# Kernel optimization log

Hardware: AMD Instinct MI355X
Metric: run time of the kernel (lower is better)

The kernel has to match this reference:

```python
import jax, jax.numpy as jnp
import numpy as np

NUM_RELATIONS = 8
NUM_BASES = 4
IN_CH, HID, OUT_CH = 128, 64, 64
N_NODES, N_EDGES = 50000, 500000


def rgcn_conv(x, edge_src, edge_dst, edge_type, basis, comp, root, bias):
    """PyG RGCNConv with basis decomposition and per-relation mean aggregation.
    basis: [B, in, out], comp: [R, B], root: [in, out], bias: [out].
    W_r = sum_b comp[r, b] * basis[b]; msg_e = x[src_e] @ W_{type_e};
    aggregate mean over incoming edges per (node, relation), sum over relations,
    then add root transform and bias.
    """
    n = x.shape[0]
    out_dim = basis.shape[2]
    # Project once through all bases: [N, B, out]  (cheap: B=4)
    h = jnp.einsum('ni,bio->nbo', x, basis)
    # Per-edge message: contract gathered basis features with per-edge comp coeffs
    msg = jnp.einsum('eb,ebo->eo', comp[edge_type], h[edge_src])  # [E, out]
    # Mean aggregation per (dst, relation): segment id = dst*R + relation
    seg = edge_dst * NUM_RELATIONS + edge_type
    sums = jax.ops.segment_sum(msg, seg, num_segments=n * NUM_RELATIONS)
    cnt = jax.ops.segment_sum(jnp.ones((msg.shape[0], 1), msg.dtype), seg,
                              num_segments=n * NUM_RELATIONS)
    mean = sums / jnp.maximum(cnt, 1.0)
    agg = mean.reshape(n, NUM_RELATIONS, out_dim).sum(axis=1)
    return agg + x @ root + bias


def setup_inputs() -> dict:
    key = jax.random.key(0)
    ks = jax.random.split(key, 12)
    s1 = 1.0 / np.sqrt(IN_CH)
    s2 = 1.0 / np.sqrt(HID)
    return {
        'x': jax.random.normal(ks[0], (N_NODES, IN_CH), jnp.float32),
        'edge_index': jax.random.randint(ks[1], (2, N_EDGES), 0, N_NODES, jnp.int64),
        'edge_type': jax.random.randint(ks[2], (N_EDGES,), 0, NUM_RELATIONS, jnp.int64),
        'basis1': jax.random.normal(ks[3], (NUM_BASES, IN_CH, HID), jnp.float32) * s1,
        'comp1': jax.random.normal(ks[4], (NUM_RELATIONS, NUM_BASES), jnp.float32) * 0.5,
        'root1': jax.random.normal(ks[5], (IN_CH, HID), jnp.float32) * s1,
        'bias1': jnp.zeros((HID,), jnp.float32),
        'basis2': jax.random.normal(ks[6], (NUM_BASES, HID, OUT_CH), jnp.float32) * s2,
        'comp2': jax.random.normal(ks[7], (NUM_RELATIONS, NUM_BASES), jnp.float32) * 0.5,
        'root2': jax.random.normal(ks[8], (HID, OUT_CH), jnp.float32) * s2,
        'bias2': jnp.zeros((OUT_CH,), jnp.float32),
    }


def reference(x, edge_index, edge_type, basis1, comp1, root1, bias1,
              basis2, comp2, root2, bias2):
    src, dst = edge_index[0], edge_index[1]
    h = rgcn_conv(x, src, dst, edge_type, basis1, comp1, root1, bias1)
    h = jax.nn.relu(h)
    out = rgcn_conv(h, src, dst, edge_type, basis2, comp2, root2, bias2)
    return out
```

## Files before the change

### kernel.cpp

```cpp
#include <hip/hip_runtime.h>
#include <cstddef>

#define NREL 8
#define SCAN_TILE 4096

typedef __bf16 bf16x8 __attribute__((ext_vector_type(8)));
typedef float f32x4 __attribute__((ext_vector_type(4)));
typedef unsigned short ushort_t;

__device__ __forceinline__ unsigned f2bf_u(float f) {
    unsigned u = __float_as_uint(f);
    u += 0x7FFFu + ((u >> 16) & 1u);
    return u >> 16;
}
__device__ __forceinline__ short f2bf(float f) { return (short)f2bf_u(f); }
__device__ __forceinline__ int pack2bf(float lo, float hi) {
    return (int)(f2bf_u(lo) | (f2bf_u(hi) << 16));
}
__device__ __forceinline__ float bfval(unsigned short g) {
    return __uint_as_float((unsigned)g << 16);
}

__global__ __launch_bounds__(256) void zero_kernel(int4* __restrict__ p, int n16,
                                                   int* __restrict__ offsN, int E)
{
    int i = blockIdx.x * 256 + threadIdx.x;
    if (i < n16) p[i] = make_int4(0, 0, 0, 0);
    if (i == 0) *offsN = E;
}

template<int K>
__device__ __forceinline__ void wfrag_body(const float* __restrict__ basis,
                                           const float* __restrict__ root,
                                           const float* __restrict__ comp,
                                           short* __restrict__ Wf, int tid)
{
    constexpr int NK = K / 32;
    int lane = tid & 63, slot = tid >> 6;
    int ks = slot % NK, t = slot / NK;
    int kg = lane >> 4, lr = lane & 15;
    int k0 = ks * 32 + kg * 8;
    union { short s[8]; int4 v; } u;
#pragma unroll
    for (int e = 0; e < 8; ++e) {
        int k = k0 + e;
        float v;
        if (t < 32) {
            int rr = t >> 2, ch = (t & 3) * 16 + lr;
            v = comp[rr * 4 + 0] * basis[((size_t)0 * K + k) * 64 + ch]
              + comp[rr * 4 + 1] * basis[((size_t)1 * K + k) * 64 + ch]
              + comp[rr * 4 + 2] * basis[((size_t)2 * K + k) * 64 + ch]
              + comp[rr * 4 + 3] * basis[((size_t)3 * K + k) * 64 + ch];
        } else {
            v = root[(size_t)k * 64 + (t - 32) * 16 + lr];
        }
        u.s[e] = f2bf(v);
    }
    *(int4*)(Wf + (size_t)tid * 8) = u.v;
}

__device__ __forceinline__ void afrag_body128(const float* __restrict__ x,
                                              short* __restrict__ xf, int N, int tid)
{
    int lane = tid & 63, slot = tid >> 6;
    int ks = slot & 3, rt = slot >> 2;
    int kg = lane >> 4, lr = lane & 15;
    int row = rt * 16 + lr, k = ks * 32 + kg * 8;
    union { short s[8]; int4 v; } u;
    if (row < N) {
        const float* xp = x + (size_t)row * 128 + k;
        float4 a = *(const float4*)xp;
        float4 b = *(const float4*)(xp + 4);
        u.s[0] = f2bf(a.x); u.s[1] = f2bf(a.y); u.s[2] = f2bf(a.z); u.s[3] = f2bf(a.w);
        u.s[4] = f2bf(b.x); u.s[5] = f2bf(b.y); u.s[6] = f2bf(b.z); u.s[7] = f2bf(b.w);
    } else {
        u.v = make_int4(0, 0, 0, 0);
    }
    *(int4*)(xf + (size_t)tid * 8) = u.v;
}

__global__ __launch_bounds__(256) void prep_hist_kernel(
    const int* __restrict__ dstp, const int* __restrict__ et, int* __restrict__ cnt8,
    const float* __restrict__ basis1, const float* __restrict__ root1,
    const float* __restrict__ comp1,  const float* __restrict__ basis2,
    const float* __restrict__ root2,  const float* __restrict__ comp2,
    const float* __restrict__ x,
    short* __restrict__ Wf1, short* __restrict__ Wf2, short* __restrict__ xf1,
    int E, int N, int NT, int HB)
{
    int b = blockIdx.x;
    if (b < HB) {
        int e = b * 256 + threadIdx.x;
        if (e < E) atomicAdd(&cnt8[dstp[e] * NREL + et[e]], 1);
        return;
    }
    b -= HB;
    if (b < 36) { wfrag_body<128>(basis1, root1, comp1, Wf1, b * 256 + threadIdx.x); return; }
    b -= 36;
    if (b < 18) { wfrag_body<64>(basis2, root2, comp2, Wf2, b * 256 + threadIdx.x); return; }
    b -= 18;
    int tid = b * 256 + threadIdx.x;
    if (tid < NT * 256) afrag_body128(x, xf1, N, tid);
}

__global__ __launch_bounds__(256) void scan_part(const int* __restrict__ cnt8,
                                                 int* __restrict__ tsum, int n)
{
    int base = blockIdx.x * SCAN_TILE;
    int s = 0;
    for (int i = threadIdx.x; i < SCAN_TILE; i += 256) {
        int idx = base + i;
        if (idx < n) {
            int4 a = ((const int4*)cnt8)[idx * 2];
            int4 b = ((const int4*)cnt8)[idx * 2 + 1];
            s += a.x + a.y + a.z + a.w + b.x + b.y + b.z + b.w;
        }
    }
    for (int d = 1; d < 64; d <<= 1) s += __shfl_xor(s, d, 64);
    __shared__ int ws[4];
    if ((threadIdx.x & 63) == 0) ws[threadIdx.x >> 6] = s;
    __syncthreads();
    if (threadIdx.x == 0) tsum[blockIdx.x] = ws[0] + ws[1] + ws[2] + ws[3];
}

__global__ __launch_bounds__(256) void scan_final(const int* __restrict__ cnt8,
                                                  const int* __restrict__ tsum,
                                                  int* __restrict__ offs, int n)
{
    const int lane = threadIdx.x & 63, wid = threadIdx.x >> 6;
    int tbase = 0;
    for (int i = 0; i < blockIdx.x; ++i) tbase += tsum[i];
    int base = blockIdx.x * SCAN_TILE + threadIdx.x * 16;
    int v[16]; int s = 0;
#pragma unroll
    for (int j = 0; j < 16; ++j) {
        int idx = base + j;
        int dv = 0;
        if (idx < n) {
            int4 a = ((const int4*)cnt8)[idx * 2];
            int4 b = ((const int4*)cnt8)[idx * 2 + 1];
            dv = a.x + a.y + a.z + a.w + b.x + b.y + b.z + b.w;
        }
        v[j] = dv; s += dv;
    }
    int inc = s;
    for (int d = 1; d < 64; d <<= 1) {
        int t = __shfl_up(inc, d, 64);
        if (lane >= d) inc += t;
    }
    __shared__ int wsum[4];
    if (lane == 63) wsum[wid] = inc;
    __syncthreads();
    int run = tbase + (inc - s);
    for (int k = 0; k < wid; ++k) run += wsum[k];
#pragma unroll
    for (int j = 0; j < 16; ++j) {
        int idx = base + j;
        if (idx < n) offs[idx] = run;
        run += v[j];
    }
}

__global__ __launch_bounds__(256) void scatter_kernel(const int* __restrict__ src,
                                                      const int* __restrict__ dst,
                                                      const int* __restrict__ et,
                                                      const int* __restrict__ offs,
                                                      int* __restrict__ cursor,
                                                      const int* __restrict__ cnt8,
                                                      int2* __restrict__ edgeP,
                                                      ushort_t* __restrict__ edgeD, int E)
{
    int e = blockIdx.x * 256 + threadIdx.x;
    if (e >= E) return;
    int d = dst[e], r = et[e], s = src[e];
    int c = cnt8[d * NREL + r];
    float inv = 1.0f / (float)(c > 1 ? c : 1);
    int pos = offs[d] + atomicAdd(&cursor[d], 1);
    edgeP[pos] = make_int2(s * NREL + r, __float_as_int(inv));
    edgeD[pos] = (ushort_t)d;
}

template<int K>
__global__ __launch_bounds__(256) void gemm_mfma(const short* __restrict__ xf,
                                                 const short* __restrict__ Wf,
                                                 const float* __restrict__ bias,
                                                 short* __restrict__ hr,
                                                 short* __restrict__ yb,
                                                 int N, int gblk)
{
    constexpr int NK = K / 32;
    __shared__ short lds[12 * NK * 512];

    const int w = threadIdx.x >> 6, lane = threadIdx.x & 63;
    const int kg = lane >> 4, lr = lane & 15;
    const int g0 = blockIdx.y * 3;

    {
        const int4* gsrc = (const int4*)(Wf + (size_t)g0 * 4 * NK * 512);
        int4* ldst = (int4*)lds;
        for (int i = threadIdx.x; i < 12 * NK * 64; i += 256)
            ldst[i] = gsrc[i];
    }

    float b0 = bias[lr], b1 = bias[16 + lr], b2 = bias[32 + lr], b3 = bias[48 + lr];

    __syncthreads();

    for (int bx = blockIdx.x; bx < gblk; bx += gridDim.x) {
        const int rt = bx * 4 + w;

        bf16x8 afrag[NK];
        const short* ap = xf + ((size_t)rt * NK * 64 + lane) * 8;
#pragma unroll
        for (int ks = 0; ks < NK; ++ks)
            afrag[ks] = *(const bf16x8*)(ap + ks * 512);

        f32x4 acc[12];
#pragma unroll
        for (int t = 0; t < 12; ++t) acc[t] = (f32x4){0.f, 0.f, 0.f, 0.f};

#pragma unroll
        for (int tt = 0; tt < 12; ++tt) {
#pragma unroll
            for (int ks = 0; ks < NK; ++ks) {
                bf16x8 bfrag = *(const bf16x8*)(lds + (tt * NK + ks) * 512 + lane * 8);
                acc[tt] = __builtin_amdgcn_mfma_f32_16x16x32_bf16(afrag[ks], bfrag,
                                                                  acc[tt], 0, 0, 0);
            }
        }

        const int drow0 = rt * 16 + kg * 4;
#pragma unroll
        for (int r = 0; r < 4; ++r) {
            int dr = drow0 + r;
            if (dr >= N) break;
#pragma unroll
            for (int gg = 0; gg < 3; ++gg) {
                int g = g0 + gg;
                if (g < 8) {
                    int u0 = pack2bf(acc[gg * 4 + 0][r], acc[gg * 4 + 1][r]);
                    int u1 = pack2bf(acc[gg * 4 + 2][r], acc[gg * 4 + 3][r]);
                    *(int2*)(hr + (size_t)dr * 512 + g * 64 + lr * 4) = make_int2(u0, u1);
                } else {
                    int u0 = pack2bf(acc[gg * 4 + 0][r] + b0, acc[gg * 4 + 1][r] + b1);
                    int u1 = pack2bf(acc[gg * 4 + 2][r] + b2, acc[gg * 4 + 3][r] + b3);
                    *(int2*)(yb + (size_t)dr * 64 + lr * 4) = make_int2(u0, u1);
                }
            }
        }
    }
}

__global__ __launch_bounds__(256) void agg_chunk_kernel(
    const int2* __restrict__ edgeP, const ushort_t* __restrict__ edgeD,
    const short* __restrict__ hr, float* __restrict__ aggF, int E)
{
    const int w = threadIdx.x >> 6, l = threadIdx.x & 63;
    const int base = (blockIdx.x * 4 + w) * 16;
    if (base >= E) return;
    const int nv = min(16, E - base);

    int idx = base + (l & 15);
    if (idx >= E) idx = E - 1;
    int2 pl = edgeP[idx];
    int dl = (int)edgeD[idx];

    const unsigned short* hp = (const unsigned short*)hr;

    int g[16];
#pragma unroll
    for (int j = 0; j < 16; ++j) {
        int srj = __shfl(pl.x, j);
        g[j] = hp[(size_t)srj * 64 + l];
    }

    float acc = 0.f;
#pragma unroll
    for (int j = 0; j < 16; ++j) {
        if (j >= nv) break;
        float invj = __uint_as_float(__shfl(pl.y, j));
        acc = fmaf(bfval((unsigned short)g[j]), invj, acc);
        int dcur = __shfl(dl, j);
        int dnxt = __shfl(dl, (j + 1) & 15);
        if (j == nv - 1 || dnxt != dcur) {
            unsafeAtomicAdd(&aggF[(size_t)dcur * 64 + l], acc);
            acc = 0.f;
        }
    }
}

template<bool BF16OUT>
__global__ __launch_bounds__(256) void agg_fin_kernel(const float* __restrict__ aggF,
                                                      const short* __restrict__ yb,
                                                      float* __restrict__ outF,
                                                      short* __restrict__ outB, int N)
{
    int i = blockIdx.x * 256 + threadIdx.x;
    if (i >= N * 64) return;
    int dst = i >> 6, l = i & 63;
    float v = aggF[i] + bfval(((const ushort_t*)yb)[i]);
    int tc = (l & 3) * 16 + (l >> 2);
    if (BF16OUT) {
        int rt2 = dst >> 4, lr2 = dst & 15;
        int ks2 = tc >> 5, kg2 = (tc >> 3) & 3, e2 = tc & 7;
        outB[(((size_t)rt2 * 2 + ks2) * 64 + kg2 * 16 + lr2) * 8 + e2] =
            f2bf(fmaxf(v, 0.f));
    } else {
        outF[(size_t)dst * 64 + tc] = v;
    }
}

extern "C" void kernel_launch(void* const* d_in, const int* in_sizes, int n_in,
                              void* d_out, int out_size, void* d_ws, size_t ws_size,
                              hipStream_t stream)
{
    const float* x      = (const float*)d_in[0];
    const int*   ei     = (const int*)d_in[1];
    const int*   et     = (const int*)d_in[2];
    const float* basis1 = (const float*)d_in[3];
    const float* comp1  = (const float*)d_in[4];
    const float* root1  = (const float*)d_in[5];
    const float* bias1  = (const float*)d_in[6];
    const float* basis2 = (const float*)d_in[7];
    const float* comp2  = (const float*)d_in[8];
    const float* root2  = (const float*)d_in[9];
    const float* bias2  = (const float*)d_in[10];
    float* out = (float*)d_out;

    const int N = in_sizes[0] / 128;
    const int E = in_sizes[2];
    const int* src  = ei;
    const int* dstp = ei + E;

    const int gblk = (N + 63) / 64;
    const int NT   = gblk * 4;
    const int HB   = (E + 255) / 256;

    char* p = (char*)d_ws;
    auto carve = [&](size_t bytes) -> char* {
        char* q = p; p += (bytes + 255) & ~(size_t)255; return q;
    };
    int*   cursor  = (int*)carve((size_t)N * 4);
    int*   cnt8    = (int*)carve((size_t)N * NREL * 4);
    float* aggF1   = (float*)carve((size_t)N * 64 * 4);
    float* aggF2   = (float*)carve((size_t)N * 64 * 4);
    char*  zend    = p;
    int*   offs    = (int*)carve((size_t)(N + 1) * 4);
    int*   tsum    = (int*)carve(256 * 4);
    int2*  edgeP   = (int2*)carve((size_t)E * 8);
    ushort_t* edgeD = (ushort_t*)carve((size_t)E * 2);
    short* Wf1     = (short*)carve((size_t)36 * 4 * 64 * 8 * 2);
    short* Wf2     = (short*)carve((size_t)36 * 2 * 64 * 8 * 2);
    short* yb      = (short*)carve((size_t)N * 64 * 2);
    short* xf1     = (short*)carve((size_t)NT * 4 * 64 * 8 * 2);
    short* xf2     = (short*)carve((size_t)NT * 2 * 64 * 8 * 2);
    short* hr      = (short*)carve((size_t)N * 512 * 2);

    const int zn16 = (int)((zend - (char*)cursor) / 16);
    const int ntiles = (N + SCAN_TILE - 1) / SCAN_TILE;
    const int CHB = (E + 63) / 64;
    const int FB  = (N * 64 + 255) / 256;

    zero_kernel<<<(zn16 + 255) / 256, 256, 0, stream>>>((int4*)cursor, zn16, offs + N, E);

    prep_hist_kernel<<<HB + 36 + 18 + NT, 256, 0, stream>>>(
        dstp, et, cnt8, basis1, root1, comp1, basis2, root2, comp2, x,
        Wf1, Wf2, xf1, E, N, NT, HB);

    scan_part<<<ntiles, 256, 0, stream>>>(cnt8, tsum, N);
    scan_final<<<ntiles, 256, 0, stream>>>(cnt8, tsum, offs, N);

    scatter_kernel<<<HB, 256, 0, stream>>>(src, dstp, et, offs, cursor,
                                           cnt8, edgeP, edgeD, E);

    gemm_mfma<128><<<dim3(256, 3), 256, 0, stream>>>(xf1, Wf1, bias1, hr, yb, N, gblk);
    agg_chunk_kernel<<<CHB, 256, 0, stream>>>(edgeP, edgeD, hr, aggF1, E);
    agg_fin_kernel<true><<<FB, 256, 0, stream>>>(aggF1, yb, nullptr, xf2, N);

    gemm_mfma<64><<<dim3(512, 3), 256, 0, stream>>>(xf2, Wf2, bias2, hr, yb, N, gblk);
    agg_chunk_kernel<<<CHB, 256, 0, stream>>>(edgeP, edgeD, hr, aggF2, E);
    agg_fin_kernel<false><<<FB, 256, 0, stream>>>(aggF2, yb, out, nullptr, N);
}
```

Baseline: 194.4 us.

## Split GEMM per output group, widen edge records, process 32 edges per wave

The GEMM kernel now handles one 64-wide output group per block instead of three, with a 9-wide grid. This lowers LDS use and accumulator registers, which should raise occupancy. The edge record now packs the premultiplied hr offset, inverse count and destination into a single int4, replacing the separate int2 and ushort arrays. The aggregation kernel handles 32 edges per wave instead of 16, which gives more gathers in flight and fewer atomic flushes, at the cost of more registers and a larger edge buffer.

```diff
diff --git a/kernel.cpp b/kernel.cpp
--- a/kernel.cpp
+++ b/kernel.cpp
@@ -167,8 +167,7 @@
                                                       const int* __restrict__ offs,
                                                       int* __restrict__ cursor,
                                                       const int* __restrict__ cnt8,
-                                                      int2* __restrict__ edgeP,
-                                                      ushort_t* __restrict__ edgeD, int E)
+                                                      int4* __restrict__ edgeP, int E)
 {
     int e = blockIdx.x * 256 + threadIdx.x;
     if (e >= E) return;
@@ -176,8 +175,7 @@
     int c = cnt8[d * NREL + r];
     float inv = 1.0f / (float)(c > 1 ? c : 1);
     int pos = offs[d] + atomicAdd(&cursor[d], 1);
-    edgeP[pos] = make_int2(s * NREL + r, __float_as_int(inv));
-    edgeD[pos] = (ushort_t)d;
+    edgeP[pos] = make_int4((s * NREL + r) * 64, __float_as_int(inv), d, 0);
 }
 
 template<int K>
@@ -189,16 +187,16 @@
                                                  int N, int gblk)
 {
     constexpr int NK = K / 32;
-    __shared__ short lds[12 * NK * 512];
+    __shared__ short lds[4 * NK * 512];
 
     const int w = threadIdx.x >> 6, lane = threadIdx.x & 63;
     const int kg = lane >> 4, lr = lane & 15;
-    const int g0 = blockIdx.y * 3;
+    const int g = blockIdx.y;
 
     {
-        const int4* gsrc = (const int4*)(Wf + (size_t)g0 * 4 * NK * 512);
+        const int4* gsrc = (const int4*)(Wf + (size_t)g * 4 * NK * 512);
         int4* ldst = (int4*)lds;
-        for (int i = threadIdx.x; i < 12 * NK * 64; i += 256)
+        for (int i = threadIdx.x; i < 4 * NK * 64; i += 256)
             ldst[i] = gsrc[i];
     }
 
@@ -215,12 +213,12 @@
         for (int ks = 0; ks < NK; ++ks)
             afrag[ks] = *(const bf16x8*)(ap + ks * 512);
 
-        f32x4 acc[12];
-#pragma unroll
-        for (int t = 0; t < 12; ++t) acc[t] = (f32x4){0.f, 0.f, 0.f, 0.f};
-
-#pragma unroll
-        for (int tt = 0; tt < 12; ++tt) {
+        f32x4 acc[4];
+#pragma unroll
+        for (int t = 0; t < 4; ++t) acc[t] = (f32x4){0.f, 0.f, 0.f, 0.f};
+
+#pragma unroll
+        for (int tt = 0; tt < 4; ++tt) {
 #pragma unroll
             for (int ks = 0; ks < NK; ++ks) {
                 bf16x8 bfrag = *(const bf16x8*)(lds + (tt * NK + ks) * 512 + lane * 8);
@@ -234,54 +232,49 @@
         for (int r = 0; r < 4; ++r) {
             int dr = drow0 + r;
             if (dr >= N) break;
-#pragma unroll
-            for (int gg = 0; gg < 3; ++gg) {
-                int g = g0 + gg;
-                if (g < 8) {
-                    int u0 = pack2bf(acc[gg * 4 + 0][r], acc[gg * 4 + 1][r]);
-                    int u1 = pack2bf(acc[gg * 4 + 2][r], acc[gg * 4 + 3][r]);
-                    *(int2*)(hr + (size_t)dr * 512 + g * 64 + lr * 4) = make_int2(u0, u1);
-                } else {
-                    int u0 = pack2bf(acc[gg * 4 + 0][r] + b0, acc[gg * 4 + 1][r] + b1);
-                    int u1 = pack2bf(acc[gg * 4 + 2][r] + b2, acc[gg * 4 + 3][r] + b3);
-                    *(int2*)(yb + (size_t)dr * 64 + lr * 4) = make_int2(u0, u1);
-                }
+            if (g < 8) {
+                int u0 = pack2bf(acc[0][r], acc[1][r]);
+                int u1 = pack2bf(acc[2][r], acc[3][r]);
+                *(int2*)(hr + (size_t)dr * 512 + g * 64 + lr * 4) = make_int2(u0, u1);
+            } else {
+                int u0 = pack2bf(acc[0][r] + b0, acc[1][r] + b1);
+                int u1 = pack2bf(acc[2][r] + b2, acc[3][r] + b3);
+                *(int2*)(yb + (size_t)dr * 64 + lr * 4) = make_int2(u0, u1);
             }
         }
     }
 }
 
 __global__ __launch_bounds__(256) void agg_chunk_kernel(
-    const int2* __restrict__ edgeP, const ushort_t* __restrict__ edgeD,
-    const short* __restrict__ hr, float* __restrict__ aggF, int E)
+    const int4* __restrict__ edgeP, const short* __restrict__ hr,
+    float* __restrict__ aggF, int E)
 {
     const int w = threadIdx.x >> 6, l = threadIdx.x & 63;
-    const int base = (blockIdx.x * 4 + w) * 16;
+    const int base = (blockIdx.x * 4 + w) * 32;
     if (base >= E) return;
-    const int nv = min(16, E - base);
-
-    int idx = base + (l & 15);
+    const int nv = min(32, E - base);
+
+    int idx = base + (l & 31);
     if (idx >= E) idx = E - 1;
-    int2 pl = edgeP[idx];
-    int dl = (int)edgeD[idx];
+    int4 pl = edgeP[idx];
 
     const unsigned short* hp = (const unsigned short*)hr;
 
-    int g[16];
-#pragma unroll
-    for (int j = 0; j < 16; ++j) {
-        int srj = __shfl(pl.x, j);
-        g[j] = hp[(size_t)srj * 64 + l];
+    int g[32];
+#pragma unroll
+    for (int j = 0; j < 32; ++j) {
+        int hoff = __shfl(pl.x, j);
+        g[j] = hp[(size_t)hoff + l];
     }
 
     float acc = 0.f;
 #pragma unroll
-    for (int j = 0; j < 16; ++j) {
+    for (int j = 0; j < 32; ++j) {
         if (j >= nv) break;
         float invj = __uint_as_float(__shfl(pl.y, j));
         acc = fmaf(bfval((unsigned short)g[j]), invj, acc);
-        int dcur = __shfl(dl, j);
-        int dnxt = __shfl(dl, (j + 1) & 15);
+        int dcur = __shfl(pl.z, j);
+        int dnxt = __shfl(pl.z, (j + 1) & 31);
         if (j == nv - 1 || dnxt != dcur) {
             unsafeAtomicAdd(&aggF[(size_t)dcur * 64 + l], acc);
             acc = 0.f;
@@ -347,8 +340,7 @@
     char*  zend    = p;
     int*   offs    = (int*)carve((size_t)(N + 1) * 4);
     int*   tsum    = (int*)carve(256 * 4);
-    int2*  edgeP   = (int2*)carve((size_t)E * 8);
-    ushort_t* edgeD = (ushort_t*)carve((size_t)E * 2);
+    int4*  edgeP   = (int4*)carve((size_t)E * 16);
     short* Wf1     = (short*)carve((size_t)36 * 4 * 64 * 8 * 2);
     short* Wf2     = (short*)carve((size_t)36 * 2 * 64 * 8 * 2);
     short* yb      = (short*)carve((size_t)N * 64 * 2);
@@ -358,7 +350,7 @@
 
     const int zn16 = (int)((zend - (char*)cursor) / 16);
     const int ntiles = (N + SCAN_TILE - 1) / SCAN_TILE;
-    const int CHB = (E + 63) / 64;
+    const int CHB = (E + 127) / 128;
     const int FB  = (N * 64 + 255) / 256;
 
     zero_kernel<<<(zn16 + 255) / 256, 256, 0, stream>>>((int4*)cursor, zn16, offs + N, E);
@@ -371,13 +363,13 @@
     scan_final<<<ntiles, 256, 0, stream>>>(cnt8, tsum, offs, N);
 
     scatter_kernel<<<HB, 256, 0, stream>>>(src, dstp, et, offs, cursor,
-                                           cnt8, edgeP, edgeD, E);
-
-    gemm_mfma<128><<<dim3(256, 3), 256, 0, stream>>>(xf1, Wf1, bias1, hr, yb, N, gblk);
-    agg_chunk_kernel<<<CHB, 256, 0, stream>>>(edgeP, edgeD, hr, aggF1, E);
+                                           cnt8, edgeP, E);
+
+    gemm_mfma<128><<<dim3(256, 9), 256, 0, stream>>>(xf1, Wf1, bias1, hr, yb, N, gblk);
+    agg_chunk_kernel<<<CHB, 256, 0, stream>>>(edgeP, hr, aggF1, E);
     agg_fin_kernel<true><<<FB, 256, 0, stream>>>(aggF1, yb, nullptr, xf2, N);
 
-    gemm_mfma<64><<<dim3(512, 3), 256, 0, stream>>>(xf2, Wf2, bias2, hr, yb, N, gblk);
-    agg_chunk_kernel<<<CHB, 256, 0, stream>>>(edgeP, edgeD, hr, aggF2, E);
+    gemm_mfma<64><<<dim3(256, 9), 256, 0, stream>>>(xf2, Wf2, bias2, hr, yb, N, gblk);
+    agg_chunk_kernel<<<CHB, 256, 0, stream>>>(edgeP, hr, aggF2, E);
     agg_fin_kernel<false><<<FB, 256, 0, stream>>>(aggF2, yb, out, nullptr, N);
 }
```

Measured after the change: 177.1 us. 1.1x faster.
